# Performance work log

Hardware: AMD Instinct MI355X
Metric: run time of the kernel (lower is better)

## Reference

```python
import jax, jax.numpy as jnp
import numpy as np

K = (3, 5, 7)
TAU_MIN, TAU_MAX = 0.03, 0.5


def _l2norm(x, axis=1, eps=1e-12):
    # matches torch F.normalize: x / max(||x||, eps)
    n = jnp.sqrt(jnp.sum(x * x, axis=axis, keepdims=True))
    return x / jnp.maximum(n, eps)


def _affinity_one(feat, kappa_ch, qw_k, kw_k, k):
    # feat: (B, C, H, W); kappa_ch: (B, 1, H, W); qw_k/kw_k: (Ca, C)
    B, C, H, W = feat.shape
    q = jnp.einsum('bchw,oc->bohw', feat, qw_k)
    key = jnp.einsum('bchw,oc->bohw', feat, kw_k)
    qn = _l2norm(q)
    kn = _l2norm(key)
    p = k // 2
    knp = jnp.pad(kn, ((0, 0), (0, 0), (p, p), (p, p)))
    # windowed cosine correlation: loop over the small fixed set of k*k offsets
    sims = []
    for dy in range(k):
        for dx in range(k):
            sims.append(jnp.sum(qn * knp[:, :, dy:dy + H, dx:dx + W], axis=1))
    sim = jnp.stack(sims, axis=1)  # (B, k*k, H, W)
    # temperature from curvature: GLOBAL min/max over the sliced channel
    kmin = kappa_ch.min()
    kmax = kappa_ch.max()
    kap_n = (kappa_ch - kmin) / (kmax - kmin + 1e-06)
    tau = jnp.clip(TAU_MAX - kap_n * (TAU_MAX - TAU_MIN), TAU_MIN, TAU_MAX)
    return sim / (tau + 1e-06)  # broadcast (B,kk,H,W) / (B,1,H,W)


def setup_inputs() -> dict:
    key = jax.random.key(0)
    k1, k2, k3, k4 = jax.random.split(key, 4)
    B, C, H, W = 4, 64, 256, 256
    CA = 32
    feat = jax.random.normal(k1, (B, C, H, W), dtype=jnp.float32)
    kappa = jax.random.uniform(k2, (B, len(K), H, W), dtype=jnp.float32)
    scale = 1.0 / np.sqrt(C)
    qw = jax.random.normal(k3, (len(K), CA, C), dtype=jnp.float32) * scale
    kw = jax.random.normal(k4, (len(K), CA, C), dtype=jnp.float32) * scale
    return {'feat': feat, 'kappa': kappa, 'qw': qw, 'kw': kw}


def reference(feat, kappa, qw, kw):
    out = []
    for i, k in enumerate(K):
        out.append(_affinity_one(feat, kappa[:, i:i + 1], qw[i], kw[i], k))
    return tuple(out)
```

## Files before the change

### kernel.cpp

```cpp
#include <hip/hip_runtime.h>
#include <stdint.h>

#define HW   65536
#define IMG  256
#define NB   4
#define NC   64
#define NA   32

typedef __attribute__((ext_vector_type(8))) short short8v;
typedef __attribute__((ext_vector_type(4))) float f32x4;

__device__ __forceinline__ unsigned short f2bf(float x) {
  unsigned u = __float_as_uint(x);
  u += 0x7FFFu + ((u >> 16) & 1u);
  return (unsigned short)(u >> 16);
}
__device__ __forceinline__ float bfval(unsigned short h) { return __uint_as_float((unsigned)h << 16); }
__device__ __forceinline__ float bflo(unsigned u) { return __uint_as_float(u << 16); }
__device__ __forceinline__ float bfhi(unsigned u) { return __uint_as_float(u & 0xFFFF0000u); }
__device__ __forceinline__ unsigned packbf(float a, float b) {
  return (unsigned)f2bf(a) | ((unsigned)f2bf(b) << 16);
}

__global__ void prep_afrag(const float* __restrict__ qw, const float* __restrict__ kw,
                           unsigned short* __restrict__ afrag, unsigned* __restrict__ mm) {
  int idx = blockIdx.x * 256 + threadIdx.x;
  if (blockIdx.x == 0 && threadIdx.x < 6)
    mm[threadIdx.x] = (threadIdx.x < 3) ? 0xFFFFFFFFu : 0u;
  if (idx >= 3 * 4 * 2 * 2 * 64 * 8) return;
  int j    = idx & 7;
  int lane = (idx >> 3) & 63;
  int h    = (idx >> 9) & 1;
  int ks   = (idx >> 10) & 1;
  int mt   = (idx >> 11) & 3;
  int i    = idx >> 13;
  int s = mt >> 1;
  int o = (mt & 1) * 16 + (lane & 15);
  int c = ks * 32 + (lane >> 4) * 8 + j;
  float v = (s ? kw : qw)[((size_t)i * NA + o) * NC + c];
  unsigned short hi = f2bf(v);
  afrag[idx] = h ? f2bf(v - bfval(hi)) : hi;
}

__global__ __launch_bounds__(256) void minmax_k(const float* __restrict__ kappa,
                                                unsigned* __restrict__ mm) {
  const int i = blockIdx.y;
  const unsigned* ku = (const unsigned*)kappa;
  unsigned lo = 0xFFFFFFFFu, hi = 0u;
  for (int idx = blockIdx.x * 256 + threadIdx.x; idx < NB * HW; idx += gridDim.x * 256) {
    int b = idx >> 16, p = idx & (HW - 1);
    unsigned v = ku[((size_t)(b * 3 + i)) * HW + p];
    lo = min(lo, v); hi = max(hi, v);
  }
#pragma unroll
  for (int d = 32; d >= 1; d >>= 1) {
    lo = min(lo, (unsigned)__shfl_xor((int)lo, d, 64));
    hi = max(hi, (unsigned)__shfl_xor((int)hi, d, 64));
  }
  __shared__ unsigned slo[4], shi[4];
  if ((threadIdx.x & 63) == 0) { slo[threadIdx.x >> 6] = lo; shi[threadIdx.x >> 6] = hi; }
  __syncthreads();
  if (threadIdx.x == 0) {
    lo = min(min(slo[0], slo[1]), min(slo[2], slo[3]));
    hi = max(max(shi[0], shi[1]), max(shi[2], shi[3]));
    atomicMin(&mm[i], lo);
    atomicMax(&mm[i + 3], hi);
  }
}

__global__ __launch_bounds__(256) void proj_all(const float* __restrict__ feat,
                                                const unsigned short* __restrict__ afr,
                                                unsigned* __restrict__ qb,
                                                unsigned* __restrict__ kb,
                                                const int nsl, const int i0) {
  const int t = blockIdx.x;
  const int b = t >> 9;
  const int p0 = (t & 511) * 128;
  const int lane = threadIdx.x & 63;
  const int w = threadIdx.x >> 6;
  const int s = w & 1;
  const int pbase = p0 + (w >> 1) * 64;

  short8v bh[4][2], bl[4][2];
  const float* fb = feat + (size_t)b * NC * HW;
#pragma unroll
  for (int nt = 0; nt < 4; ++nt) {
    const int px = pbase + nt * 16 + (lane & 15);
#pragma unroll
    for (int ks = 0; ks < 2; ++ks) {
      const float* fp = fb + (size_t)(ks * 32 + (lane >> 4) * 8) * HW + px;
      float fv[8];
#pragma unroll
      for (int j = 0; j < 8; ++j) fv[j] = fp[(size_t)j * HW];
#pragma unroll
      for (int j = 0; j < 8; ++j) {
        unsigned short h = f2bf(fv[j]);
        bh[nt][ks][j] = (short)h;
        bl[nt][ks][j] = (short)f2bf(fv[j] - bfval(h));
      }
    }
  }

  unsigned* dstbuf0 = s ? kb : qb;

#pragma unroll 1
  for (int sl = 0; sl < nsl; ++sl) {
    const unsigned short* af = afr + (size_t)(i0 + sl) * 8192;

    short8v ah[2][2], al[2][2];
#pragma unroll
    for (int m = 0; m < 2; ++m)
#pragma unroll
      for (int ks = 0; ks < 2; ++ks) {
        int mt = s * 2 + m;
        const unsigned short* base = af + (size_t)((mt * 2 + ks) * 2) * 512 + lane * 8;
        ah[m][ks] = *(const short8v*)(base);
        al[m][ks] = *(const short8v*)(base + 512);
      }

    f32x4 acc[2][4];
#pragma unroll
    for (int m = 0; m < 2; ++m)
#pragma unroll
      for (int nt = 0; nt < 4; ++nt) acc[m][nt] = (f32x4){0.f, 0.f, 0.f, 0.f};

#pragma unroll
    for (int nt = 0; nt < 4; ++nt)
#pragma unroll
      for (int ks = 0; ks < 2; ++ks)
#pragma unroll
        for (int m = 0; m < 2; ++m) {
          acc[m][nt] = __builtin_amdgcn_mfma_f32_16x16x32_bf16(ah[m][ks], bh[nt][ks], acc[m][nt], 0, 0, 0);
          acc[m][nt] = __builtin_amdgcn_mfma_f32_16x16x32_bf16(ah[m][ks], bl[nt][ks], acc[m][nt], 0, 0, 0);
          acc[m][nt] = __builtin_amdgcn_mfma_f32_16x16x32_bf16(al[m][ks], bh[nt][ks], acc[m][nt], 0, 0, 0);
        }

    unsigned* dstbuf = dstbuf0 + (size_t)sl * NB * HW * 16;
#pragma unroll
    for (int nt = 0; nt < 4; ++nt) {
      float ssq = 0.f;
#pragma unroll
      for (int m = 0; m < 2; ++m)
#pragma unroll
        for (int r = 0; r < 4; ++r) ssq = fmaf(acc[m][nt][r], acc[m][nt][r], ssq);
      ssq += __shfl_xor(ssq, 16, 64);
      ssq += __shfl_xor(ssq, 32, 64);
      float inv = 1.0f / fmaxf(sqrtf(ssq), 1e-12f);
      const int px = pbase + nt * 16 + (lane & 15);
      const size_t pix = (size_t)b * HW + px;
#pragma unroll
      for (int m = 0; m < 2; ++m) {
        int c0 = m * 16 + (lane >> 4) * 4;
        uint2 v;
        v.x = packbf(acc[m][nt][0] * inv, acc[m][nt][1] * inv);
        v.y = packbf(acc[m][nt][2] * inv, acc[m][nt][3] * inv);
        *(uint2*)(dstbuf + pix * 16 + (c0 >> 1)) = v;
      }
    }
  }
}

template <int KS>
__device__ __forceinline__ void corr_body(unsigned* __restrict__ ksh,
                                          const unsigned* __restrict__ qn,
                                          const unsigned* __restrict__ kn,
                                          const float* __restrict__ kappa,
                                          const unsigned* __restrict__ mm,
                                          const int i, const int b,
                                          float* __restrict__ out) {
  constexpr int P = KS / 2;
  constexpr int TX = 16 + 2 * P;
  constexpr int NPX = TX * TX;
  constexpr int KK = KS * KS;
  constexpr int LS = 17;

  const int y0 = blockIdx.y * 16, x0 = blockIdx.x * 16;
  const int tx = threadIdx.x, ty = threadIdx.y;
  const int tid = ty * 16 + tx;

  for (int px = tid; px < NPX; px += 256) {
    int ry = px / TX;
    int gy = y0 - P + ry;
    int gx = x0 - P + (px - ry * TX);
    uint4 v0, v1, v2, v3;
    if ((unsigned)gy < (unsigned)IMG && (unsigned)gx < (unsigned)IMG) {
      const uint4* sp = (const uint4*)(kn + ((size_t)b * HW + gy * IMG + gx) * 16);
      v0 = sp[0]; v1 = sp[1]; v2 = sp[2]; v3 = sp[3];
    } else {
      v0 = make_uint4(0u, 0u, 0u, 0u); v1 = v0; v2 = v0; v3 = v0;
    }
    unsigned* d = ksh + px * LS;
    d[0] = v0.x;  d[1] = v0.y;  d[2] = v0.z;  d[3] = v0.w;
    d[4] = v1.x;  d[5] = v1.y;  d[6] = v1.z;  d[7] = v1.w;
    d[8] = v2.x;  d[9] = v2.y;  d[10] = v2.z; d[11] = v2.w;
    d[12] = v3.x; d[13] = v3.y; d[14] = v3.z; d[15] = v3.w;
  }

  const int y = y0 + ty, x = x0 + tx;
  const size_t pix = (size_t)b * HW + y * IMG + x;
  float q[NA];
  {
    const uint4* sp = (const uint4*)(qn + pix * 16);
    uint4 v0 = sp[0], v1 = sp[1], v2 = sp[2], v3 = sp[3];
    unsigned u[16] = {v0.x, v0.y, v0.z, v0.w, v1.x, v1.y, v1.z, v1.w,
                      v2.x, v2.y, v2.z, v2.w, v3.x, v3.y, v3.z, v3.w};
#pragma unroll
    for (int t = 0; t < 16; ++t) { q[2 * t] = bflo(u[t]); q[2 * t + 1] = bfhi(u[t]); }
  }

  float kap = kappa[((size_t)(b * 3 + i)) * HW + y * IMG + x];
  float kmin = __uint_as_float(mm[i]);
  float kmax = __uint_as_float(mm[i + 3]);
  float kapn = (kap - kmin) / (kmax - kmin + 1e-6f);
  float tau = fminf(fmaxf(0.5f - kapn * (0.5f - 0.03f), 0.03f), 0.5f);
  float scale = 1.0f / (tau + 1e-6f);

  __syncthreads();

  float* ob = out + (size_t)b * KK * HW + y * IMG + x;
#pragma unroll 1
  for (int dy = 0; dy < KS; ++dy) {
#pragma unroll
    for (int dx = 0; dx < KS; ++dx) {
      const unsigned* kr = ksh + ((ty + dy) * TX + (tx + dx)) * LS;
      float s = 0.f;
#pragma unroll
      for (int t = 0; t < 16; ++t) {
        unsigned u = kr[t];
        s = fmaf(q[2 * t], bflo(u), s);
        s = fmaf(q[2 * t + 1], bfhi(u), s);
      }
      ob[(size_t)(dy * KS + dx) * HW] = s * scale;
    }
  }
}

__global__ __launch_bounds__(256) void corr_all(const unsigned* __restrict__ qb,
                                                const unsigned* __restrict__ kb,
                                                const float* __restrict__ kappa,
                                                const unsigned* __restrict__ mm,
                                                const int i0, float* __restrict__ out) {
  __shared__ unsigned ksh[8228];
  const int sl = blockIdx.z >> 2;
  const int b = blockIdx.z & 3;
  const int i = i0 + sl;
  const unsigned* qn = qb + (size_t)sl * NB * HW * 16;
  const unsigned* kn = kb + (size_t)sl * NB * HW * 16;
  const size_t plane = (size_t)NB * HW;
  if (i == 0)
    corr_body<3>(ksh, qn, kn, kappa, mm, 0, b, out);
  else if (i == 1)
    corr_body<5>(ksh, qn, kn, kappa, mm, 1, b, out + plane * 9);
  else
    corr_body<7>(ksh, qn, kn, kappa, mm, 2, b, out + plane * 34);
}

extern "C" void kernel_launch(void* const* d_in, const int* in_sizes, int n_in,
                              void* d_out, int out_size, void* d_ws, size_t ws_size,
                              hipStream_t stream) {
  const float* feat  = (const float*)d_in[0];
  const float* kappa = (const float*)d_in[1];
  const float* qw    = (const float*)d_in[2];
  const float* kw    = (const float*)d_in[3];
  float* out = (float*)d_out;

  char* ws = (char*)d_ws;
  unsigned* mm = (unsigned*)ws;
  unsigned short* afrag = (unsigned short*)(ws + 64);
  unsigned* qbuf = (unsigned*)(ws + 65536);

  const size_t slot = (size_t)NB * HW * 16;
  const size_t need3 = 65536 + (size_t)6 * slot * 4;
  const int fused = (ws_size >= need3) ? 1 : 0;
  const int nsl = fused ? 3 : 1;
  unsigned* kbuf = qbuf + (size_t)nsl * slot;

  hipLaunchKernelGGL(prep_afrag, dim3(96), dim3(256), 0, stream, qw, kw, afrag, mm);
  hipLaunchKernelGGL(minmax_k, dim3(64, 3), dim3(256), 0, stream, kappa, mm);

  if (fused) {
    hipLaunchKernelGGL(proj_all, dim3(NB * HW / 128), dim3(256), 0, stream,
                       feat, afrag, qbuf, kbuf, 3, 0);
    hipLaunchKernelGGL(corr_all, dim3(IMG / 16, IMG / 16, NB * 3), dim3(16, 16), 0, stream,
                       qbuf, kbuf, kappa, mm, 0, out);
  } else {
    for (int i = 0; i < 3; ++i) {
      hipLaunchKernelGGL(proj_all, dim3(NB * HW / 128), dim3(256), 0, stream,
                         feat, afrag, qbuf, kbuf, 1, i);
      hipLaunchKernelGGL(corr_all, dim3(IMG / 16, IMG / 16, NB), dim3(16, 16), 0, stream,
                         qbuf, kbuf, kappa, mm, i, out);
    }
  }
}
```

Baseline: 119.6 us.

## Compute windowed correlation with bf16 MFMA tiles instead of scalar dot products

The correlation kernel now issues 16x16x32 bf16 MFMAs between each query row tile and a 32-wide key row strip for every dy. It writes the 16x32 result matrices to shared memory and reads back only the diagonal band needed for each dx offset. This replaces the per-thread scalar FMA loop over a shared key halo and trades wasted MFMA work on unused off-diagonal entries for much higher matrix throughput. Keys are now read straight from global memory per row rather than staged in LDS. The projection kernel's feature loads are also regrouped so all 32 loads per ks are issued before conversion, to raise memory-level parallelism.

```diff
diff --git a/kernel.cpp b/kernel.cpp
--- a/kernel.cpp
+++ b/kernel.cpp
@@ -16,8 +16,6 @@
   return (unsigned short)(u >> 16);
 }
 __device__ __forceinline__ float bfval(unsigned short h) { return __uint_as_float((unsigned)h << 16); }
-__device__ __forceinline__ float bflo(unsigned u) { return __uint_as_float(u << 16); }
-__device__ __forceinline__ float bfhi(unsigned u) { return __uint_as_float(u & 0xFFFF0000u); }
 __device__ __forceinline__ unsigned packbf(float a, float b) {
   return (unsigned)f2bf(a) | ((unsigned)f2bf(b) << 16);
 }
@@ -84,21 +82,24 @@
   short8v bh[4][2], bl[4][2];
   const float* fb = feat + (size_t)b * NC * HW;
 #pragma unroll
-  for (int nt = 0; nt < 4; ++nt) {
-    const int px = pbase + nt * 16 + (lane & 15);
-#pragma unroll
-    for (int ks = 0; ks < 2; ++ks) {
+  for (int ks = 0; ks < 2; ++ks) {
+    float fv[32];
+#pragma unroll
+    for (int nt = 0; nt < 4; ++nt) {
+      const int px = pbase + nt * 16 + (lane & 15);
       const float* fp = fb + (size_t)(ks * 32 + (lane >> 4) * 8) * HW + px;
-      float fv[8];
-#pragma unroll
-      for (int j = 0; j < 8; ++j) fv[j] = fp[(size_t)j * HW];
+#pragma unroll
+      for (int j = 0; j < 8; ++j) fv[nt * 8 + j] = fp[(size_t)j * HW];
+    }
+#pragma unroll
+    for (int nt = 0; nt < 4; ++nt)
 #pragma unroll
       for (int j = 0; j < 8; ++j) {
-        unsigned short h = f2bf(fv[j]);
+        float f = fv[nt * 8 + j];
+        unsigned short h = f2bf(f);
         bh[nt][ks][j] = (short)h;
-        bl[nt][ks][j] = (short)f2bf(fv[j] - bfval(h));
-      }
-    }
+        bl[nt][ks][j] = (short)f2bf(f - bfval(h));
+      }
   }
 
   unsigned* dstbuf0 = s ? kb : qb;
@@ -161,76 +162,66 @@
 }
 
 template <int KS>
-__device__ __forceinline__ void corr_body(unsigned* __restrict__ ksh,
-                                          const unsigned* __restrict__ qn,
-                                          const unsigned* __restrict__ kn,
-                                          const float* __restrict__ kappa,
-                                          const unsigned* __restrict__ mm,
-                                          const int i, const int b,
-                                          float* __restrict__ out) {
+__device__ __forceinline__ void corr_mfma_body(float* __restrict__ Csh,
+                                               const unsigned* __restrict__ qn,
+                                               const unsigned* __restrict__ kn,
+                                               const float* __restrict__ kappa,
+                                               const unsigned* __restrict__ mm,
+                                               const int i, const int b,
+                                               float* __restrict__ out) {
   constexpr int P = KS / 2;
-  constexpr int TX = 16 + 2 * P;
-  constexpr int NPX = TX * TX;
   constexpr int KK = KS * KS;
-  constexpr int LS = 17;
-
   const int y0 = blockIdx.y * 16, x0 = blockIdx.x * 16;
-  const int tx = threadIdx.x, ty = threadIdx.y;
-  const int tid = ty * 16 + tx;
-
-  for (int px = tid; px < NPX; px += 256) {
-    int ry = px / TX;
-    int gy = y0 - P + ry;
-    int gx = x0 - P + (px - ry * TX);
-    uint4 v0, v1, v2, v3;
-    if ((unsigned)gy < (unsigned)IMG && (unsigned)gx < (unsigned)IMG) {
-      const uint4* sp = (const uint4*)(kn + ((size_t)b * HW + gy * IMG + gx) * 16);
-      v0 = sp[0]; v1 = sp[1]; v2 = sp[2]; v3 = sp[3];
-    } else {
-      v0 = make_uint4(0u, 0u, 0u, 0u); v1 = v0; v2 = v0; v3 = v0;
-    }
-    unsigned* d = ksh + px * LS;
-    d[0] = v0.x;  d[1] = v0.y;  d[2] = v0.z;  d[3] = v0.w;
-    d[4] = v1.x;  d[5] = v1.y;  d[6] = v1.z;  d[7] = v1.w;
-    d[8] = v2.x;  d[9] = v2.y;  d[10] = v2.z; d[11] = v2.w;
-    d[12] = v3.x; d[13] = v3.y; d[14] = v3.z; d[15] = v3.w;
-  }
-
-  const int y = y0 + ty, x = x0 + tx;
-  const size_t pix = (size_t)b * HW + y * IMG + x;
-  float q[NA];
-  {
-    const uint4* sp = (const uint4*)(qn + pix * 16);
-    uint4 v0 = sp[0], v1 = sp[1], v2 = sp[2], v3 = sp[3];
-    unsigned u[16] = {v0.x, v0.y, v0.z, v0.w, v1.x, v1.y, v1.z, v1.w,
-                      v2.x, v2.y, v2.z, v2.w, v3.x, v3.y, v3.z, v3.w};
-#pragma unroll
-    for (int t = 0; t < 16; ++t) { q[2 * t] = bflo(u[t]); q[2 * t + 1] = bfhi(u[t]); }
-  }
-
-  float kap = kappa[((size_t)(b * 3 + i)) * HW + y * IMG + x];
+  const int lane = threadIdx.x & 63, w = threadIdx.x >> 6;
+  const int cq = lane & 15;
+  const int rq = lane >> 4;
+  const int y = y0 + w * 4 + rq;
+  const int x = x0 + cq;
+
+  float* Cw = Csh + w * 2592;
+
+  short8v A[4];
+#pragma unroll
+  for (int yl = 0; yl < 4; ++yl) {
+    const unsigned* p = qn + ((size_t)b * HW + (size_t)(y0 + w * 4 + yl) * IMG + x0 + cq) * 16 + rq * 4;
+    A[yl] = *(const short8v*)p;
+  }
+
+  float kap = kappa[((size_t)(b * 3 + i)) * HW + (size_t)y * IMG + x];
   float kmin = __uint_as_float(mm[i]);
   float kmax = __uint_as_float(mm[i + 3]);
   float kapn = (kap - kmin) / (kmax - kmin + 1e-6f);
   float tau = fminf(fmaxf(0.5f - kapn * (0.5f - 0.03f), 0.03f), 0.5f);
   float scale = 1.0f / (tau + 1e-6f);
 
-  __syncthreads();
-
-  float* ob = out + (size_t)b * KK * HW + y * IMG + x;
+  const int kx0 = x0 - P + cq;
+  const int kx1 = kx0 + 16;
+
 #pragma unroll 1
   for (int dy = 0; dy < KS; ++dy) {
+    __syncthreads();
+#pragma unroll
+    for (int yl = 0; yl < 4; ++yl) {
+      const int ky = y0 + w * 4 + yl + dy - P;
+      f32x4 a0 = {0.f, 0.f, 0.f, 0.f}, a1 = {0.f, 0.f, 0.f, 0.f};
+      if ((unsigned)ky < (unsigned)IMG) {
+        const unsigned* krow = kn + ((size_t)b * HW + (size_t)ky * IMG) * 16;
+        short8v B0 = {0, 0, 0, 0, 0, 0, 0, 0};
+        short8v B1 = {0, 0, 0, 0, 0, 0, 0, 0};
+        if ((unsigned)kx0 < (unsigned)IMG) B0 = *(const short8v*)(krow + (size_t)kx0 * 16 + rq * 4);
+        if ((unsigned)kx1 < (unsigned)IMG) B1 = *(const short8v*)(krow + (size_t)kx1 * 16 + rq * 4);
+        a0 = __builtin_amdgcn_mfma_f32_16x16x32_bf16(A[yl], B0, a0, 0, 0, 0);
+        a1 = __builtin_amdgcn_mfma_f32_16x16x32_bf16(A[yl], B1, a1, 0, 0, 0);
+      }
+      *(f32x4*)(Cw + yl * 648 + cq * 20 + rq * 4) = a0;
+      *(f32x4*)(Cw + yl * 648 + (16 + cq) * 20 + rq * 4) = a1;
+    }
+    __syncthreads();
+    float* ob = out + ((size_t)b * KK + (size_t)dy * KS) * HW + (size_t)y * IMG + x;
 #pragma unroll
     for (int dx = 0; dx < KS; ++dx) {
-      const unsigned* kr = ksh + ((ty + dy) * TX + (tx + dx)) * LS;
-      float s = 0.f;
-#pragma unroll
-      for (int t = 0; t < 16; ++t) {
-        unsigned u = kr[t];
-        s = fmaf(q[2 * t], bflo(u), s);
-        s = fmaf(q[2 * t + 1], bfhi(u), s);
-      }
-      ob[(size_t)(dy * KS + dx) * HW] = s * scale;
+      float v = Cw[rq * 648 + (cq + dx) * 20 + cq];
+      ob[(size_t)dx * HW] = v * scale;
     }
   }
 }
@@ -240,7 +231,7 @@
                                                 const float* __restrict__ kappa,
                                                 const unsigned* __restrict__ mm,
                                                 const int i0, float* __restrict__ out) {
-  __shared__ unsigned ksh[8228];
+  __shared__ __align__(16) float Csh[10368];
   const int sl = blockIdx.z >> 2;
   const int b = blockIdx.z & 3;
   const int i = i0 + sl;
@@ -248,11 +239,11 @@
   const unsigned* kn = kb + (size_t)sl * NB * HW * 16;
   const size_t plane = (size_t)NB * HW;
   if (i == 0)
-    corr_body<3>(ksh, qn, kn, kappa, mm, 0, b, out);
+    corr_mfma_body<3>(Csh, qn, kn, kappa, mm, 0, b, out);
   else if (i == 1)
-    corr_body<5>(ksh, qn, kn, kappa, mm, 1, b, out + plane * 9);
+    corr_mfma_body<5>(Csh, qn, kn, kappa, mm, 1, b, out + plane * 9);
   else
-    corr_body<7>(ksh, qn, kn, kappa, mm, 2, b, out + plane * 34);
+    corr_mfma_body<7>(Csh, qn, kn, kappa, mm, 2, b, out + plane * 34);
 }
 
 extern "C" void kernel_launch(void* const* d_in, const int* in_sizes, int n_in,
@@ -281,13 +272,13 @@
   if (fused) {
     hipLaunchKernelGGL(proj_all, dim3(NB * HW / 128), dim3(256), 0, stream,
                        feat, afrag, qbuf, kbuf, 3, 0);
-    hipLaunchKernelGGL(corr_all, dim3(IMG / 16, IMG / 16, NB * 3), dim3(16, 16), 0, stream,
+    hipLaunchKernelGGL(corr_all, dim3(IMG / 16, IMG / 16, NB * 3), dim3(256), 0, stream,
                        qbuf, kbuf, kappa, mm, 0, out);
   } else {
     for (int i = 0; i < 3; ++i) {
       hipLaunchKernelGGL(proj_all, dim3(NB * HW / 128), dim3(256), 0, stream,
                          feat, afrag, qbuf, kbuf, 1, i);
-      hipLaunchKernelGGL(corr_all, dim3(IMG / 16, IMG / 16, NB), dim3(16, 16), 0, stream,
+      hipLaunchKernelGGL(corr_all, dim3(IMG / 16, IMG / 16, NB), dim3(256), 0, stream,
                          qbuf, kbuf, kappa, mm, i, out);
     }
   }
```

Result: slower. 122.9 us (+2.7%).
